# Kernel optimization log

Hardware: AMD Instinct MI355X
Metric: run time of the kernel (lower is better)

The kernel has to match this reference:

```python
import jax, jax.numpy as jnp
import numpy as np

B, T, IN, H, L, NC = 256, 512, 34, 80, 10, 5


def setup_inputs() -> dict:
    key = jax.random.key(0)
    ks = jax.random.split(key, 8)
    s = 0.1  # keep gates out of hard saturation
    return {
        "x": jax.random.normal(ks[0], (B, T, IN), jnp.float32),
        "W_ih0": jax.random.normal(ks[1], (4 * H, IN), jnp.float32) * s,
        "W_ih_rest": jax.random.normal(ks[2], (L - 1, 4 * H, H), jnp.float32) * s,
        "W_hh": jax.random.normal(ks[3], (L, 4 * H, H), jnp.float32) * s,
        "b_ih": jax.random.normal(ks[4], (L, 4 * H), jnp.float32) * s,
        "b_hh": jax.random.normal(ks[5], (L, 4 * H), jnp.float32) * s,
        "fc_w": jax.random.normal(ks[6], (NC, H), jnp.float32) * s,
        "fc_b": jax.random.normal(ks[7], (NC,), jnp.float32) * s,
    }


def _lstm_layer(xseq, Wih, Whh, bih, bhh):
    # xseq: [B, T, in]; PyTorch gate order (i, f, g, o) along the 4H axis.
    Bb = xseq.shape[0]
    Hh = Whh.shape[1]
    # Precompute input projections for all timesteps (one big GEMM).
    xp = jnp.einsum('bti,gi->btg', xseq, Wih) + bih + bhh  # [B, T, 4H]
    xp = jnp.swapaxes(xp, 0, 1)  # [T, B, 4H] for scan over time

    def step(carry, xt):
        h, c = carry
        gates = xt + h @ Whh.T  # [B, 4H]
        i, f, g, o = jnp.split(gates, 4, axis=-1)
        i = jax.nn.sigmoid(i)
        f = jax.nn.sigmoid(f)
        g = jnp.tanh(g)
        o = jax.nn.sigmoid(o)
        c = f * c + i * g
        h = o * jnp.tanh(c)
        return (h, c), h

    h0 = jnp.zeros((Bb, Hh), xseq.dtype)
    _, hs = jax.lax.scan(step, (h0, h0), xp)  # hs: [T, B, H]
    return jnp.swapaxes(hs, 0, 1)  # [B, T, H]


def reference(x, W_ih0, W_ih_rest, W_hh, b_ih, b_hh, fc_w, fc_b):
    # 10-layer stacked LSTM (eval mode: inter-layer dropout disabled).
    h = _lstm_layer(x, W_ih0, W_hh[0], b_ih[0], b_hh[0])
    for l in range(1, L):
        h = _lstm_layer(h, W_ih_rest[l - 1], W_hh[l], b_ih[l], b_hh[l])
    # fc on last timestep's hidden state
    return h[:, -1, :] @ fc_w.T + fc_b  # [B, NC]
```

## Files before the change

kernel.cpp:

```cpp
#include <hip/hip_runtime.h>

#define B_   256
#define T_   512
#define IN_  34
#define H_   80
#define L_   10
#define NC_  5
#define G4   320
#define NG   3
#define TPB  (NG * G4)
#define HPS  96

typedef _Float16 h2 __attribute__((ext_vector_type(2)));

template <int CTRL>
__device__ __forceinline__ float dpp_mov(float v) {
    return __int_as_float(__builtin_amdgcn_update_dpp(0, __float_as_int(v), CTRL, 0xF, 0xF, true));
}
__device__ __forceinline__ h2 bc(unsigned u) { return __builtin_bit_cast(h2, u); }

__global__ void prep_kernel(const float* __restrict__ Wih0, const float* __restrict__ WihR,
                            const float* __restrict__ Whh,  const float* __restrict__ bih,
                            const float* __restrict__ bhh,
                            unsigned* __restrict__ w, float* __restrict__ bbuf) {
    int idx = blockIdx.x * 256 + threadIdx.x;
    const int ND = L_ * 20 * G4 * 4;
    if (idx < ND) {
        int c    = idx & 3;
        int lane = (idx >> 2) % G4;
        int n    = ((idx >> 2) / G4) % 20;
        int l    = (idx >> 2) / (G4 * 20);
        int j = n * 4 + c;
        int gate = j / 20, q = j % 20;
        int e = lane >> 2, q4 = lane & 3;
        int row = gate * H_ + e;
        int kk = 40 * q4 + 2 * q;
        float a, bvl;
        if (kk < H_) {
            if (l == 0) {
                a   = (kk     < IN_) ? Wih0[row * IN_ + kk]     : 0.f;
                bvl = (kk + 1 < IN_) ? Wih0[row * IN_ + kk + 1] : 0.f;
            } else {
                const float* p = WihR + ((size_t)(l - 1) * G4 + row) * H_;
                a = p[kk]; bvl = p[kk + 1];
            }
        } else {
            const float* p = Whh + ((size_t)l * G4 + row) * H_;
            a = p[kk - H_]; bvl = p[kk - H_ + 1];
        }
        h2 pa; pa[0] = (_Float16)a; pa[1] = (_Float16)bvl;
        w[idx] = __builtin_bit_cast(unsigned, pa);
    }
    if (idx < L_ * G4) bbuf[idx] = bih[idx] + bhh[idx];
}

__global__ __launch_bounds__(TPB, 1) void lstm_stack_kernel(
    const float* __restrict__ x,
    const uint4* __restrict__ w,
    const float* __restrict__ bbuf,
    const float* __restrict__ fcw,
    const float* __restrict__ fcb,
    float* __restrict__ out)
{
    const int b    = blockIdx.x;
    const int tid  = threadIdx.x;
    const int grp  = tid / G4;
    const int lane = tid - grp * G4;
    const int e    = lane >> 2;
    const int q4   = lane & 3;
    const int eS   = (e / 40) * 48 + (e % 40);

    const float mA  = (q4 == 2) ? -2.885390082f : -1.442695041f;
    const float bA  = (q4 == 2) ? 2.f : 1.f;
    const float cA0 = (q4 == 2) ? -1.f : 0.f;
    const bool  sel1 = (q4 & 1) != 0;
    const bool  sel2 = (q4 & 2) != 0;

    __shared__ __align__(16) _Float16 hist[T_][HPS];
    __shared__ __align__(16) _Float16 ring[2][2][HPS];
    __shared__ __align__(16) _Float16 hss[NG][2][HPS];

    for (int j = tid; j < T_ * H_; j += TPB) {
        int t = j / H_, k = j % H_;
        float v = (k < IN_) ? x[((size_t)b * T_ + t) * IN_ + k] : 0.f;
        hist[t][(k / 40) * 48 + (k % 40)] = (_Float16)v;
    }

    _Float16 hfin = (_Float16)0.f;

    for (int pass = 0; pass < 4; ++pass) {
        const int l = NG * pass + grp;
        const bool activeL = (l < L_);
        const int lc = activeL ? l : 0;

        const uint4* wp = w + (size_t)lc * 20 * G4 + lane;
        uint4 U0 = wp[0 * G4],  U1 = wp[1 * G4],  U2 = wp[2 * G4],  U3 = wp[3 * G4],  U4 = wp[4 * G4];
        uint4 U5 = wp[5 * G4],  U6 = wp[6 * G4],  U7 = wp[7 * G4],  U8 = wp[8 * G4],  U9 = wp[9 * G4];
        uint4 U10 = wp[10 * G4], U11 = wp[11 * G4], U12 = wp[12 * G4], U13 = wp[13 * G4], U14 = wp[14 * G4];
        uint4 U15 = wp[15 * G4], U16 = wp[16 * G4], U17 = wp[17 * G4], U18 = wp[18 * G4], U19 = wp[19 * G4];
        const float bias = bbuf[lc * G4 + q4 * H_ + e];

        if (tid < 288) ((unsigned*)hss)[tid] = 0;
        __syncthreads();

        float cold = 0.f;

#pragma unroll 2
        for (int tick = 0; tick <= T_ + 1; ++tick) {
            const int tau = tick - grp;
            if (activeL && tau >= 0 && tau < T_) {
                const int par = tau & 1;
                const uint4* src;
                if (q4 < 2) src = (grp == 0) ? (const uint4*)(&hist[tau][48 * q4])
                                             : (const uint4*)(&ring[grp - 1][par][48 * q4]);
                else        src = (const uint4*)(&hss[grp][par][48 * (q4 - 2)]);
                uint4 M0 = src[0], M1 = src[1], M2 = src[2], M3 = src[3], M4 = src[4];
                h2 p0 = bc(M0.x), p1 = bc(M0.y), p2 = bc(M0.z), p3 = bc(M0.w);
                h2 p4 = bc(M1.x), p5 = bc(M1.y), p6 = bc(M1.z), p7 = bc(M1.w);
                h2 p8 = bc(M2.x), p9 = bc(M2.y), p10 = bc(M2.z), p11 = bc(M2.w);
                h2 p12 = bc(M3.x), p13 = bc(M3.y), p14 = bc(M3.z), p15 = bc(M3.w);
                h2 p16 = bc(M4.x), p17 = bc(M4.y), p18 = bc(M4.z), p19 = bc(M4.w);

                float aI = 0.f, aF = 0.f, aG = 0.f, aO = 0.f;
#define D(acc, W, C, P) acc = __builtin_amdgcn_fdot2(bc(W.C), P, acc, false);
                D(aI, U0, x, p0)  D(aI, U0, y, p1)  D(aI, U0, z, p2)  D(aI, U0, w, p3)
                D(aI, U1, x, p4)  D(aI, U1, y, p5)  D(aI, U1, z, p6)  D(aI, U1, w, p7)
                D(aI, U2, x, p8)  D(aI, U2, y, p9)  D(aI, U2, z, p10) D(aI, U2, w, p11)
                D(aI, U3, x, p12) D(aI, U3, y, p13) D(aI, U3, z, p14) D(aI, U3, w, p15)
                D(aI, U4, x, p16) D(aI, U4, y, p17) D(aI, U4, z, p18) D(aI, U4, w, p19)
                D(aF, U5, x, p0)  D(aF, U5, y, p1)  D(aF, U5, z, p2)  D(aF, U5, w, p3)
                D(aF, U6, x, p4)  D(aF, U6, y, p5)  D(aF, U6, z, p6)  D(aF, U6, w, p7)
                D(aF, U7, x, p8)  D(aF, U7, y, p9)  D(aF, U7, z, p10) D(aF, U7, w, p11)
                D(aF, U8, x, p12) D(aF, U8, y, p13) D(aF, U8, z, p14) D(aF, U8, w, p15)
                D(aF, U9, x, p16) D(aF, U9, y, p17) D(aF, U9, z, p18) D(aF, U9, w, p19)
                D(aG, U10, x, p0)  D(aG, U10, y, p1)  D(aG, U10, z, p2)  D(aG, U10, w, p3)
                D(aG, U11, x, p4)  D(aG, U11, y, p5)  D(aG, U11, z, p6)  D(aG, U11, w, p7)
                D(aG, U12, x, p8)  D(aG, U12, y, p9)  D(aG, U12, z, p10) D(aG, U12, w, p11)
                D(aG, U13, x, p12) D(aG, U13, y, p13) D(aG, U13, z, p14) D(aG, U13, w, p15)
                D(aG, U14, x, p16) D(aG, U14, y, p17) D(aG, U14, z, p18) D(aG, U14, w, p19)
                D(aO, U15, x, p0)  D(aO, U15, y, p1)  D(aO, U15, z, p2)  D(aO, U15, w, p3)
                D(aO, U16, x, p4)  D(aO, U16, y, p5)  D(aO, U16, z, p6)  D(aO, U16, w, p7)
                D(aO, U17, x, p8)  D(aO, U17, y, p9)  D(aO, U17, z, p10) D(aO, U17, w, p11)
                D(aO, U18, x, p12) D(aO, U18, y, p13) D(aO, U18, z, p14) D(aO, U18, w, p15)
                D(aO, U19, x, p16) D(aO, U19, y, p17) D(aO, U19, z, p18) D(aO, U19, w, p19)
#undef D
                float kI = sel1 ? aF : aI, oI = sel1 ? aI : aF;
                float AIF = kI + dpp_mov<0xB1>(oI);
                float kG = sel1 ? aO : aG, oG = sel1 ? aG : aO;
                float BGO = kG + dpp_mov<0xB1>(oG);
                float k2v = sel2 ? BGO : AIF, o2 = sel2 ? AIF : BGO;
                float S = k2v + dpp_mov<0x4E>(o2) + bias;

                float y   = __builtin_amdgcn_rcpf(1.f + __builtin_amdgcn_exp2f(mA * S));
                float act = __builtin_fmaf(bA, y, cA0);
                float t2v  = dpp_mov<0x4E>(act);
                float prod = act * t2v;
                float t3v  = dpp_mov<0xB1>(prod);
                float cnew = __builtin_fmaf(act, cold, t3v);
                float th   = __builtin_fmaf(2.f,
                               __builtin_amdgcn_rcpf(1.f + __builtin_amdgcn_exp2f(-2.885390082f * cnew)),
                               -1.f);
                float h = t2v * th;
                cold = cnew;

                if (q4 == 1) {
                    _Float16 h16 = (_Float16)h;
                    hss[grp][par ^ 1][eS] = h16;
                    if (grp == 2) hist[tau][eS] = h16;
                    else          ring[grp][par][eS] = h16;
                    hfin = h16;
                }
            }
            __syncthreads();
        }
    }

    if (grp == 0 && q4 == 1) hist[T_ - 1][eS] = hfin;
    __syncthreads();
    if (tid < NC_) {
        float acc = fcb[tid];
#pragma unroll
        for (int j = 0; j < H_; ++j)
            acc += fcw[tid * H_ + j] * (float)hist[T_ - 1][(j / 40) * 48 + (j % 40)];
        out[b * NC_ + tid] = acc;
    }
}

extern "C" void kernel_launch(void* const* d_in, const int* in_sizes, int n_in,
                              void* d_out, int out_size, void* d_ws, size_t ws_size,
                              hipStream_t stream) {
    const float* x    = (const float*)d_in[0];
    const float* Wih0 = (const float*)d_in[1];
    const float* WihR = (const float*)d_in[2];
    const float* Whh  = (const float*)d_in[3];
    const float* bih  = (const float*)d_in[4];
    const float* bhh  = (const float*)d_in[5];
    const float* fcw  = (const float*)d_in[6];
    const float* fcb  = (const float*)d_in[7];

    unsigned* w  = (unsigned*)d_ws;
    float* bbuf  = (float*)(w + 256000);

    prep_kernel<<<dim3(1000), dim3(256), 0, stream>>>(
        Wih0, WihR, Whh, bih, bhh, w, bbuf);

    lstm_stack_kernel<<<dim3(B_), dim3(TPB), 0, stream>>>(
        x, (const uint4*)w, bbuf, fcw, fcb, (float*)d_out);
}
```

Before: 1.840 ms.

## Split last LSTM layer into input-projection producer and recurrent-chain consumer

The original fourth pass ran only layer 10 on one group of the 3-group wavefront, which left the other groups idle while that group did the full input-plus-recurrent dot product every step. Now only three full passes run. Layer 10 is handled separately: one thread group precomputes the input projection two timesteps ahead into a shared ring buffer, and another group runs only the recurrent half of the dot product plus the gate math. This shortens the serial per-step critical path for the last layer. In exchange it adds a second packed weight buffer, extra shared memory, and still one block-wide barrier per timestep.

After: 1.777 ms. 1.04x faster.

```diff
diff --git a/kernel.cpp b/kernel.cpp
--- a/kernel.cpp
+++ b/kernel.cpp
@@ -22,7 +22,8 @@
 __global__ void prep_kernel(const float* __restrict__ Wih0, const float* __restrict__ WihR,
                             const float* __restrict__ Whh,  const float* __restrict__ bih,
                             const float* __restrict__ bhh,
-                            unsigned* __restrict__ w, float* __restrict__ bbuf) {
+                            unsigned* __restrict__ w, float* __restrict__ bbuf,
+                            unsigned* __restrict__ tw) {
     int idx = blockIdx.x * 256 + threadIdx.x;
     const int ND = L_ * 20 * G4 * 4;
     if (idx < ND) {
@@ -51,12 +52,26 @@
         h2 pa; pa[0] = (_Float16)a; pa[1] = (_Float16)bvl;
         w[idx] = __builtin_bit_cast(unsigned, pa);
     }
+    if (idx < 2 * 10 * G4 * 4) {
+        int c = idx & 3, u4 = idx >> 2;
+        int lane = u4 % G4, n = (u4 / G4) % 10, side = u4 / (G4 * 10);
+        int j = n * 4 + c;
+        int gate = j / 10, q = j % 10;
+        int e = lane >> 2, q4 = lane & 3;
+        int row = gate * H_ + e;
+        int k0 = 20 * q4 + 2 * q;
+        const float* p = (side == 0) ? WihR + ((size_t)8 * G4 + row) * H_
+                                     : Whh  + ((size_t)9 * G4 + row) * H_;
+        h2 pa; pa[0] = (_Float16)p[k0]; pa[1] = (_Float16)p[k0 + 1];
+        tw[idx] = __builtin_bit_cast(unsigned, pa);
+    }
     if (idx < L_ * G4) bbuf[idx] = bih[idx] + bhh[idx];
 }
 
 __global__ __launch_bounds__(TPB, 1) void lstm_stack_kernel(
     const float* __restrict__ x,
     const uint4* __restrict__ w,
+    const uint4* __restrict__ tw,
     const float* __restrict__ bbuf,
     const float* __restrict__ fcw,
     const float* __restrict__ fcb,
@@ -69,6 +84,7 @@
     const int e    = lane >> 2;
     const int q4   = lane & 3;
     const int eS   = (e / 40) * 48 + (e % 40);
+    const int eS24 = (e / 20) * 24 + (e % 20);
 
     const float mA  = (q4 == 2) ? -2.885390082f : -1.442695041f;
     const float bA  = (q4 == 2) ? 2.f : 1.f;
@@ -79,6 +95,8 @@
     __shared__ __align__(16) _Float16 hist[T_][HPS];
     __shared__ __align__(16) _Float16 ring[2][2][HPS];
     __shared__ __align__(16) _Float16 hss[NG][2][HPS];
+    __shared__ __align__(16) float xp[4][4][84];
+    __shared__ __align__(16) _Float16 hs9[2][4][24];
 
     for (int j = tid; j < T_ * H_; j += TPB) {
         int t = j / H_, k = j % H_;
@@ -86,19 +104,15 @@
         hist[t][(k / 40) * 48 + (k % 40)] = (_Float16)v;
     }
 
-    _Float16 hfin = (_Float16)0.f;
-
-    for (int pass = 0; pass < 4; ++pass) {
+    for (int pass = 0; pass < 3; ++pass) {
         const int l = NG * pass + grp;
-        const bool activeL = (l < L_);
-        const int lc = activeL ? l : 0;
-
-        const uint4* wp = w + (size_t)lc * 20 * G4 + lane;
+
+        const uint4* wp = w + (size_t)l * 20 * G4 + lane;
         uint4 U0 = wp[0 * G4],  U1 = wp[1 * G4],  U2 = wp[2 * G4],  U3 = wp[3 * G4],  U4 = wp[4 * G4];
         uint4 U5 = wp[5 * G4],  U6 = wp[6 * G4],  U7 = wp[7 * G4],  U8 = wp[8 * G4],  U9 = wp[9 * G4];
         uint4 U10 = wp[10 * G4], U11 = wp[11 * G4], U12 = wp[12 * G4], U13 = wp[13 * G4], U14 = wp[14 * G4];
         uint4 U15 = wp[15 * G4], U16 = wp[16 * G4], U17 = wp[17 * G4], U18 = wp[18 * G4], U19 = wp[19 * G4];
-        const float bias = bbuf[lc * G4 + q4 * H_ + e];
+        const float bias = bbuf[l * G4 + q4 * H_ + e];
 
         if (tid < 288) ((unsigned*)hss)[tid] = 0;
         __syncthreads();
@@ -108,7 +122,7 @@
 #pragma unroll 2
         for (int tick = 0; tick <= T_ + 1; ++tick) {
             const int tau = tick - grp;
-            if (activeL && tau >= 0 && tau < T_) {
+            if (tau >= 0 && tau < T_) {
                 const int par = tau & 1;
                 const uint4* src;
                 if (q4 < 2) src = (grp == 0) ? (const uint4*)(&hist[tau][48 * q4])
@@ -168,15 +182,123 @@
                     hss[grp][par ^ 1][eS] = h16;
                     if (grp == 2) hist[tau][eS] = h16;
                     else          ring[grp][par][eS] = h16;
-                    hfin = h16;
                 }
             }
             __syncthreads();
         }
     }
 
-    if (grp == 0 && q4 == 1) hist[T_ - 1][eS] = hfin;
-    __syncthreads();
+    {
+        const bool isChain = tid < G4;
+        const bool isProd  = (tid >= G4) && (tid < 2 * G4);
+        const uint4* twp = tw + (size_t)(isChain ? 1 : 0) * 10 * G4 + lane;
+        uint4 V0 = twp[0 * G4], V1 = twp[1 * G4], V2 = twp[2 * G4], V3 = twp[3 * G4], V4 = twp[4 * G4];
+        uint4 V5 = twp[5 * G4], V6 = twp[6 * G4], V7 = twp[7 * G4], V8 = twp[8 * G4], V9 = twp[9 * G4];
+        const float bias9 = bbuf[9 * G4 + q4 * H_ + e];
+
+        if (tid < 96) ((unsigned*)hs9)[tid] = 0;
+
+        float cold9 = 0.f;
+        _Float16 h9 = (_Float16)0.f;
+
+#define TDOTS(SPTR)                                                                  \
+    const uint2* sp_ = (const uint2*)(SPTR);                                         \
+    uint2 TA_ = sp_[0], TB_ = sp_[1], TC_ = sp_[2], TD_ = sp_[3], TE_ = sp_[4];      \
+    h2 p0 = bc(TA_.x), p1 = bc(TA_.y), p2 = bc(TB_.x), p3 = bc(TB_.y);               \
+    h2 p4 = bc(TC_.x), p5 = bc(TC_.y), p6 = bc(TD_.x), p7 = bc(TD_.y);               \
+    h2 p8 = bc(TE_.x), p9 = bc(TE_.y);                                               \
+    float aI = 0.f, aF = 0.f, aG = 0.f, aO = 0.f;                                    \
+    aI = __builtin_amdgcn_fdot2(bc(V0.x), p0, aI, false);                            \
+    aI = __builtin_amdgcn_fdot2(bc(V0.y), p1, aI, false);                            \
+    aI = __builtin_amdgcn_fdot2(bc(V0.z), p2, aI, false);                            \
+    aI = __builtin_amdgcn_fdot2(bc(V0.w), p3, aI, false);                            \
+    aI = __builtin_amdgcn_fdot2(bc(V1.x), p4, aI, false);                            \
+    aI = __builtin_amdgcn_fdot2(bc(V1.y), p5, aI, false);                            \
+    aI = __builtin_amdgcn_fdot2(bc(V1.z), p6, aI, false);                            \
+    aI = __builtin_amdgcn_fdot2(bc(V1.w), p7, aI, false);                            \
+    aI = __builtin_amdgcn_fdot2(bc(V2.x), p8, aI, false);                            \
+    aI = __builtin_amdgcn_fdot2(bc(V2.y), p9, aI, false);                            \
+    aF = __builtin_amdgcn_fdot2(bc(V2.z), p0, aF, false);                            \
+    aF = __builtin_amdgcn_fdot2(bc(V2.w), p1, aF, false);                            \
+    aF = __builtin_amdgcn_fdot2(bc(V3.x), p2, aF, false);                            \
+    aF = __builtin_amdgcn_fdot2(bc(V3.y), p3, aF, false);                            \
+    aF = __builtin_amdgcn_fdot2(bc(V3.z), p4, aF, false);                            \
+    aF = __builtin_amdgcn_fdot2(bc(V3.w), p5, aF, false);                            \
+    aF = __builtin_amdgcn_fdot2(bc(V4.x), p6, aF, false);                            \
+    aF = __builtin_amdgcn_fdot2(bc(V4.y), p7, aF, false);                            \
+    aF = __builtin_amdgcn_fdot2(bc(V4.z), p8, aF, false);                            \
+    aF = __builtin_amdgcn_fdot2(bc(V4.w), p9, aF, false);                            \
+    aG = __builtin_amdgcn_fdot2(bc(V5.x), p0, aG, false);                            \
+    aG = __builtin_amdgcn_fdot2(bc(V5.y), p1, aG, false);                            \
+    aG = __builtin_amdgcn_fdot2(bc(V5.z), p2, aG, false);                            \
+    aG = __builtin_amdgcn_fdot2(bc(V5.w), p3, aG, false);                            \
+    aG = __builtin_amdgcn_fdot2(bc(V6.x), p4, aG, false);                            \
+    aG = __builtin_amdgcn_fdot2(bc(V6.y), p5, aG, false);                            \
+    aG = __builtin_amdgcn_fdot2(bc(V6.z), p6, aG, false);                            \
+    aG = __builtin_amdgcn_fdot2(bc(V6.w), p7, aG, false);                            \
+    aG = __builtin_amdgcn_fdot2(bc(V7.x), p8, aG, false);                            \
+    aG = __builtin_amdgcn_fdot2(bc(V7.y), p9, aG, false);                            \
+    aO = __builtin_amdgcn_fdot2(bc(V7.z), p0, aO, false);                            \
+    aO = __builtin_amdgcn_fdot2(bc(V7.w), p1, aO, false);                            \
+    aO = __builtin_amdgcn_fdot2(bc(V8.x), p2, aO, false);                            \
+    aO = __builtin_amdgcn_fdot2(bc(V8.y), p3, aO, false);                            \
+    aO = __builtin_amdgcn_fdot2(bc(V8.z), p4, aO, false);                            \
+    aO = __builtin_amdgcn_fdot2(bc(V8.w), p5, aO, false);                            \
+    aO = __builtin_amdgcn_fdot2(bc(V9.x), p6, aO, false);                            \
+    aO = __builtin_amdgcn_fdot2(bc(V9.y), p7, aO, false);                            \
+    aO = __builtin_amdgcn_fdot2(bc(V9.z), p8, aO, false);                            \
+    aO = __builtin_amdgcn_fdot2(bc(V9.w), p9, aO, false);                            \
+    float kI = sel1 ? aF : aI, oI = sel1 ? aI : aF;                                  \
+    float AIF = kI + dpp_mov<0xB1>(oI);                                              \
+    float kG = sel1 ? aO : aG, oG = sel1 ? aG : aO;                                  \
+    float BGO = kG + dpp_mov<0xB1>(oG);                                              \
+    float k2v = sel2 ? BGO : AIF, o2 = sel2 ? AIF : BGO;                             \
+    float S = k2v + dpp_mov<0x4E>(o2);
+
+#define TPRODUCE(TP) {                                                               \
+    TDOTS(&hist[TP][q4 * 20 + (q4 >= 2 ? 8 : 0)])                                    \
+    xp[(TP) & 3][q4][e] = S + bias9;                                                 \
+}
+
+        for (int pp = 0; pp < 2; ++pp) {
+            __syncthreads();
+            if (isProd) { TPRODUCE(pp) }
+        }
+        __syncthreads();
+
+#pragma unroll 2
+        for (int t = 0; t < T_; ++t) {
+            if (isProd) {
+                int tp = t + 2;
+                if (tp < T_) { TPRODUCE(tp) }
+            } else if (isChain) {
+                const int par = t & 1;
+                TDOTS(&hs9[par][q4][0])
+                S += xp[t & 3][q4][e];
+
+                float y   = __builtin_amdgcn_rcpf(1.f + __builtin_amdgcn_exp2f(mA * S));
+                float act = __builtin_fmaf(bA, y, cA0);
+                float t2v  = dpp_mov<0x4E>(act);
+                float prod = act * t2v;
+                float t3v  = dpp_mov<0xB1>(prod);
+                float cnew = __builtin_fmaf(act, cold9, t3v);
+                float th   = __builtin_fmaf(2.f,
+                               __builtin_amdgcn_rcpf(1.f + __builtin_amdgcn_exp2f(-2.885390082f * cnew)),
+                               -1.f);
+                float h = t2v * th;
+                cold9 = cnew;
+                h9 = (_Float16)h;
+                if (q4 == 1) hs9[par ^ 1][0][eS24] = h9;
+            }
+            __syncthreads();
+        }
+#undef TPRODUCE
+#undef TDOTS
+
+        if (isChain && q4 == 1) hist[T_ - 1][eS] = h9;
+        __syncthreads();
+    }
+
     if (tid < NC_) {
         float acc = fcb[tid];
 #pragma unroll
@@ -200,10 +322,11 @@
 
     unsigned* w  = (unsigned*)d_ws;
     float* bbuf  = (float*)(w + 256000);
+    unsigned* tw = (unsigned*)(bbuf + 3200);
 
     prep_kernel<<<dim3(1000), dim3(256), 0, stream>>>(
-        Wih0, WihR, Whh, bih, bhh, w, bbuf);
+        Wih0, WihR, Whh, bih, bhh, w, bbuf, tw);
 
     lstm_stack_kernel<<<dim3(B_), dim3(TPB), 0, stream>>>(
-        x, (const uint4*)w, bbuf, fcw, fcb, (float*)d_out);
-}
+        x, (const uint4*)w, (const uint4*)tw, bbuf, fcw, fcb, (float*)d_out);
+}
```
